# Optimization experiments

Measured on AMD Instinct MI355X. Metric: run time of the kernel, lower is better.

The kernel has to match this reference:

```python
import jax, jax.numpy as jnp
import numpy as np

B, N, K, D, H = 8, 128, 64, 256, 8  # batch, groups, keys-per-query, k_dim (=h_size), n_head


def setup_inputs() -> dict:
    key = jax.random.key(0)
    kq, kk, kv, kw, kb = jax.random.split(key, 5)
    bound = 1.0 / np.sqrt(D)  # torch nn.Bilinear default init bound
    return {
        "q": jax.random.normal(kq, (B, N, 1, D), jnp.float32),
        "k": jax.random.normal(kk, (B, N, K, D), jnp.float32),
        "v": jax.random.normal(kv, (B, N, K, D), jnp.float32),
        "W": jax.random.uniform(kw, (H, D, D), jnp.float32, -bound, bound),
        "b": jax.random.uniform(kb, (H,), jnp.float32, -bound, bound),
    }


def reference(q, k, v, W, b):
    Bs, Ns, Ks, Ds = k.shape
    Hh = W.shape[0]
    qe = q[:, :, 0, :]  # (B,N,D); torch expands q over K, einsum broadcasts instead
    # nn.Bilinear: scores[b,n,k,h] = q[b,n,:] @ W[h] @ k[b,n,k,:] + b[h]
    scores = jnp.einsum('bnd,hde,bnke->bnkh', qe, W, k) + b  # (B,N,K,H)
    # Faithful to torch's .view(B, N, -1, K): row-major reinterpretation of the
    # trailing (K, H) pair as (H, K) — a dim-mixing reshape, not a transpose.
    attn = scores.reshape(Bs, Ns, Hh, Ks)
    attn = jax.nn.softmax(attn, axis=-1)  # softmax over last dim (dropout p=0)
    # matmul(attn, v) -> (B,N,H,Dv); then sum over the head axis
    output = jnp.einsum('bnhk,bnkd->bnd', attn, v)
    return output, attn
```

## Files before the change

kernel.cpp:

```cpp
#include <hip/hip_runtime.h>
#include <math.h>

namespace {

constexpr int D = 256;
constexpr int H = 8;

typedef __attribute__((ext_vector_type(8))) short bf16x8;
typedef __attribute__((ext_vector_type(4))) float f32x4;

__device__ inline unsigned short bf16rn(float x) {
  unsigned u = __builtin_bit_cast(unsigned, x);
  u += 0x7fffu + ((u >> 16) & 1u);
  return (unsigned short)(u >> 16);
}
__device__ inline float bf16tof(unsigned short b) {
  return __builtin_bit_cast(float, (unsigned)b << 16);
}

constexpr size_t OFF_QW  = 0;
constexpr size_t OFF_WFH = (size_t)8 << 20;
constexpr size_t OFF_WFL = (size_t)9 << 20;
constexpr size_t OFF_QFH = (size_t)10 << 20;
constexpr size_t OFF_QFL = ((size_t)10 << 20) + ((size_t)512 << 10);

__global__ __launch_bounds__(256) void prep_kernel(
    const float* __restrict__ q, const float* __restrict__ W,
    char* __restrict__ ws) {
  const int gid = blockIdx.x * 256 + threadIdx.x;
  float e[8];
  char *hi_base, *lo_base;
  size_t outoff;
  if (gid < 65536) {
    const int l = gid & 63, ks = (gid >> 6) & 7, he = gid >> 9;
    const int h = he >> 4, et = he & 15;
    const int d0 = ks * 32 + ((l >> 4) << 3);
    const int ecol = et * 16 + (l & 15);
    const float* src = W + (size_t)h * 65536 + (size_t)d0 * 256 + ecol;
    #pragma unroll
    for (int j = 0; j < 8; ++j) e[j] = src[j * 256];
    hi_base = ws + OFF_WFH; lo_base = ws + OFF_WFL;
    outoff = (size_t)gid * 16;
  } else {
    const int t = gid - 65536;
    const int l = t & 63, ks = (t >> 6) & 7, bt = t >> 9;
    const int row = bt * 16 + (l & 15);
    const int d0 = ks * 32 + ((l >> 4) << 3);
    const float4* src = reinterpret_cast<const float4*>(q + (size_t)row * 256 + d0);
    float4 a = src[0], b = src[1];
    e[0] = a.x; e[1] = a.y; e[2] = a.z; e[3] = a.w;
    e[4] = b.x; e[5] = b.y; e[6] = b.z; e[7] = b.w;
    hi_base = ws + OFF_QFH; lo_base = ws + OFF_QFL;
    outoff = (size_t)t * 16;
  }
  unsigned hw[4], lw[4];
  #pragma unroll
  for (int p = 0; p < 4; ++p) {
    unsigned short h0 = bf16rn(e[2 * p]), h1 = bf16rn(e[2 * p + 1]);
    unsigned short l0 = bf16rn(e[2 * p] - bf16tof(h0));
    unsigned short l1 = bf16rn(e[2 * p + 1] - bf16tof(h1));
    hw[p] = (unsigned)h0 | ((unsigned)h1 << 16);
    lw[p] = (unsigned)l0 | ((unsigned)l1 << 16);
  }
  *reinterpret_cast<uint4*>(hi_base + outoff) = make_uint4(hw[0], hw[1], hw[2], hw[3]);
  *reinterpret_cast<uint4*>(lo_base + outoff) = make_uint4(lw[0], lw[1], lw[2], lw[3]);
}

__global__ __launch_bounds__(256) void qw_mfma_kernel(
    const char* __restrict__ ws_in, float* __restrict__ qW) {
  const int tid = threadIdx.x;
  const int w   = blockIdx.x * 4 + (tid >> 6);
  const int l   = tid & 63;
  const int bng = w >> 5;
  const int heg = w & 31;
  const char* qfh = ws_in + OFF_QFH;
  const char* qfl = ws_in + OFF_QFL;
  const char* wfh = ws_in + OFF_WFH;
  const char* wfl = ws_in + OFF_WFL;

  f32x4 acc[2][4];
  #pragma unroll
  for (int i = 0; i < 2; ++i)
    #pragma unroll
    for (int j = 0; j < 4; ++j) acc[i][j] = {0.f, 0.f, 0.f, 0.f};

  #pragma unroll 2
  for (int ks = 0; ks < 8; ++ks) {
    bf16x8 aH[2], aL[2], bH[4], bL[4];
    #pragma unroll
    for (int i = 0; i < 2; ++i) {
      const size_t off = ((size_t)((bng * 2 + i) * 8 + ks) * 64 + l) * 16;
      aH[i] = *reinterpret_cast<const bf16x8*>(qfh + off);
      aL[i] = *reinterpret_cast<const bf16x8*>(qfl + off);
    }
    #pragma unroll
    for (int j = 0; j < 4; ++j) {
      const size_t off = ((size_t)((heg * 4 + j) * 8 + ks) * 64 + l) * 16;
      bH[j] = *reinterpret_cast<const bf16x8*>(wfh + off);
      bL[j] = *reinterpret_cast<const bf16x8*>(wfl + off);
    }
    #pragma unroll
    for (int i = 0; i < 2; ++i)
      #pragma unroll
      for (int j = 0; j < 4; ++j) {
        acc[i][j] = __builtin_amdgcn_mfma_f32_16x16x32_bf16(aH[i], bH[j], acc[i][j], 0, 0, 0);
        acc[i][j] = __builtin_amdgcn_mfma_f32_16x16x32_bf16(aH[i], bL[j], acc[i][j], 0, 0, 0);
        acc[i][j] = __builtin_amdgcn_mfma_f32_16x16x32_bf16(aL[i], bH[j], acc[i][j], 0, 0, 0);
      }
  }

  const int rbase = (l >> 4) * 4;
  const int col   = l & 15;
  #pragma unroll
  for (int i = 0; i < 2; ++i)
    #pragma unroll
    for (int j = 0; j < 4; ++j) {
      const size_t cidx = (size_t)(heg * 4 + j) * 16 + col;
      #pragma unroll
      for (int r = 0; r < 4; ++r) {
        const int bn = (bng * 2 + i) * 16 + rbase + r;
        qW[(size_t)bn * 2048 + cidx] = acc[i][j][r];
      }
    }
}

constexpr int FA_HI = 0;
constexpr int FA_LO = 16640;
constexpr int FB_HI = 33280;
constexpr int FB_LO = 41600;
constexpr int SMEM_BYTES = 49920;

__global__ __launch_bounds__(256) void score_kernel(
    const float* __restrict__ qW, const float* __restrict__ kin,
    const float* __restrict__ bin, float* __restrict__ attn_out) {
  __shared__ alignas(16) long long smem_ll[SMEM_BYTES / 8];
  char* sm = reinterpret_cast<char*>(smem_ll);
  const int tid = threadIdx.x;
  const int bn  = blockIdx.x;
  const int kh  = blockIdx.y;
  const int wid = tid >> 6;
  const int ln  = tid & 63;

  const float4* k4 = reinterpret_cast<const float4*>(kin) +
                     (size_t)bn * 4096 + (size_t)kh * 2048;
  float4 kv[8];
  #pragma unroll
  for (int i = 0; i < 8; ++i) kv[i] = k4[tid + 256 * i];
  const float4* qw4 = reinterpret_cast<const float4*>(qW) + (size_t)bn * 512;
  float4 qv0 = qw4[tid];
  float4 qv1 = qw4[tid + 256];

  {
    const uint4 z = make_uint4(0u, 0u, 0u, 0u);
    #pragma unroll
    for (int i = 0; i < 2; ++i) {
      int idx = tid + 256 * i;
      int region = idx >> 8;
      int rem = idx & 255;
      int ks = rem >> 5, slot = 32 + (rem & 31);
      int off = (region ? FB_LO : FB_HI) + ks * 1040 + slot * 16;
      *reinterpret_cast<uint4*>(sm + off) = z;
    }
  }

  #pragma unroll
  for (int i = 0; i < 8; ++i) {
    int quad = tid + 256 * i;
    int row = quad >> 6, equad = quad & 63;
    int tile = row >> 4, lrow = row & 15;
    int ks = equad >> 3, g = (equad >> 1) & 3, j0 = (equad & 1) * 4;
    int base = tile * 8320 + ks * 1040 + (lrow * 4 + g) * 16 + j0 * 2;
    float e[4] = {kv[i].x, kv[i].y, kv[i].z, kv[i].w};
    unsigned short h0 = bf16rn(e[0]), h1 = bf16rn(e[1]),
                   h2 = bf16rn(e[2]), h3 = bf16rn(e[3]);
    unsigned short l0 = bf16rn(e[0] - bf16tof(h0)), l1 = bf16rn(e[1] - bf16tof(h1)),
                   l2 = bf16rn(e[2] - bf16tof(h2)), l3 = bf16rn(e[3] - bf16tof(h3));
    uint2 hw = make_uint2((unsigned)h0 | ((unsigned)h1 << 16),
                          (unsigned)h2 | ((unsigned)h3 << 16));
    uint2 lw = make_uint2((unsigned)l0 | ((unsigned)l1 << 16),
                          (unsigned)l2 | ((unsigned)l3 << 16));
    *reinterpret_cast<uint2*>(sm + FA_HI + base) = hw;
    *reinterpret_cast<uint2*>(sm + FA_LO + base) = lw;
  }
  #pragma unroll
  for (int i = 0; i < 2; ++i) {
    int p = tid + 256 * i;
    int hh = p >> 6, equad = p & 63;
    int ks = equad >> 3, g = (equad >> 1) & 3, j0 = (equad & 1) * 4;
    int base = ks * 1040 + (hh * 4 + g) * 16 + j0 * 2;
    float4 qv = i == 0 ? qv0 : qv1;
    float e[4] = {qv.x, qv.y, qv.z, qv.w};
    unsigned short h0 = bf16rn(e[0]), h1 = bf16rn(e[1]),
                   h2 = bf16rn(e[2]), h3 = bf16rn(e[3]);
    unsigned short l0 = bf16rn(e[0] - bf16tof(h0)), l1 = bf16rn(e[1] - bf16tof(h1)),
                   l2 = bf16rn(e[2] - bf16tof(h2)), l3 = bf16rn(e[3] - bf16tof(h3));
    uint2 hw = make_uint2((unsigned)h0 | ((unsigned)h1 << 16),
                          (unsigned)h2 | ((unsigned)h3 << 16));
    uint2 lw = make_uint2((unsigned)l0 | ((unsigned)l1 << 16),
                          (unsigned)l2 | ((unsigned)l3 << 16));
    *reinterpret_cast<uint2*>(sm + FB_HI + base) = hw;
    *reinterpret_cast<uint2*>(sm + FB_LO + base) = lw;
  }
  __syncthreads();
  if (wid >= 2) return;

  const int T = wid;
  const int slot_r = (ln & 15) * 4 + (ln >> 4);
  const char* paH = sm + FA_HI + T * 8320 + slot_r * 16;
  const char* paL = sm + FA_LO + T * 8320 + slot_r * 16;
  const char* pbH = sm + FB_HI + slot_r * 16;
  const char* pbL = sm + FB_LO + slot_r * 16;
  f32x4 acc = {0.f, 0.f, 0.f, 0.f};
  #pragma unroll
  for (int ks = 0; ks < 8; ++ks) {
    bf16x8 aH = *reinterpret_cast<const bf16x8*>(paH + ks * 1040);
    bf16x8 aL = *reinterpret_cast<const bf16x8*>(paL + ks * 1040);
    bf16x8 bH = *reinterpret_cast<const bf16x8*>(pbH + ks * 1040);
    bf16x8 bL = *reinterpret_cast<const bf16x8*>(pbL + ks * 1040);
    acc = __builtin_amdgcn_mfma_f32_16x16x32_bf16(aH, bH, acc, 0, 0, 0);
    acc = __builtin_amdgcn_mfma_f32_16x16x32_bf16(aH, bL, acc, 0, 0, 0);
    acc = __builtin_amdgcn_mfma_f32_16x16x32_bf16(aL, bH, acc, 0, 0, 0);
  }

  const int col = ln & 15;
  const bool valid = col < 8;
  const float bias = bin[ln & 7];
  float x0 = acc[0] + bias, x1 = acc[1] + bias, x2 = acc[2] + bias, x3 = acc[3] + bias;
  float m = valid ? fmaxf(fmaxf(x0, x1), fmaxf(x2, x3)) : -1e30f;
  m = fmaxf(m, __shfl_xor(m, 1, 64));
  m = fmaxf(m, __shfl_xor(m, 2, 64));
  m = fmaxf(m, __shfl_xor(m, 4, 64));
  m = fmaxf(m, __shfl_xor(m, 16, 64));
  float e0 = valid ? expf(x0 - m) : 0.f;
  float e1 = valid ? expf(x1 - m) : 0.f;
  float e2 = valid ? expf(x2 - m) : 0.f;
  float e3 = valid ? expf(x3 - m) : 0.f;
  float s = e0 + e1 + e2 + e3;
  s += __shfl_xor(s, 1, 64);
  s += __shfl_xor(s, 2, 64);
  s += __shfl_xor(s, 4, 64);
  s += __shfl_xor(s, 16, 64);
  if (valid) {
    float inv = 1.f / s;
    size_t base = (size_t)bn * 512 + (size_t)(kh * 32 + T * 16 + (ln >> 4) * 4) * 8 + col;
    attn_out[base]      = e0 * inv;
    attn_out[base + 8]  = e1 * inv;
    attn_out[base + 16] = e2 * inv;
    attn_out[base + 24] = e3 * inv;
  }
}

__global__ __launch_bounds__(256) void pv_kernel(
    const float* __restrict__ vin, const float* __restrict__ attn_in,
    float* __restrict__ out) {
  __shared__ float wpart[4][64];
  __shared__ float wsum[64];
  __shared__ float s_red[4][260];
  const int tid = threadIdx.x;
  const int bn  = blockIdx.x;
  const int wid = tid >> 6;
  const int ln  = tid & 63;

  float a0 = attn_in[(size_t)bn * 512 + tid];
  float a1 = attn_in[(size_t)bn * 512 + 256 + tid];
  wpart[wid][ln] = a0 + a1;
  __syncthreads();
  if (tid < 64) wsum[tid] = wpart[0][tid] + wpart[1][tid] + wpart[2][tid] + wpart[3][tid];
  __syncthreads();

  const float4* v4 = reinterpret_cast<const float4*>(vin) + (size_t)bn * 4096;
  float4 acc = make_float4(0.f, 0.f, 0.f, 0.f);
  #pragma unroll 8
  for (int i = 0; i < 16; ++i) {
    const int r = wid + 4 * i;
    float w = wsum[r];
    float4 vv = v4[r * 64 + ln];
    acc.x += w * vv.x; acc.y += w * vv.y; acc.z += w * vv.z; acc.w += w * vv.w;
  }
  *reinterpret_cast<float4*>(&s_red[wid][ln << 2]) = acc;
  __syncthreads();

  out[(size_t)bn * D + tid] =
      s_red[0][tid] + s_red[1][tid] + s_red[2][tid] + s_red[3][tid];
}

}

extern "C" void kernel_launch(void* const* d_in, const int* in_sizes, int n_in,
                              void* d_out, int out_size, void* d_ws, size_t ws_size,
                              hipStream_t stream) {
  const float* q = (const float*)d_in[0];
  const float* k = (const float*)d_in[1];
  const float* v = (const float*)d_in[2];
  const float* W = (const float*)d_in[3];
  const float* b = (const float*)d_in[4];

  float* out  = (float*)d_out;
  float* attn = out + 262144;
  char*  ws   = (char*)d_ws;
  float* qWbuf = (float*)(ws + OFF_QW);

  hipLaunchKernelGGL(prep_kernel,    dim3(384), dim3(256), 0, stream, q, W, ws);
  hipLaunchKernelGGL(qw_mfma_kernel, dim3(256), dim3(256), 0, stream, ws, qWbuf);
  hipLaunchKernelGGL(score_kernel,   dim3(1024, 2), dim3(256), 0, stream,
                     qWbuf, k, b, attn);
  hipLaunchKernelGGL(pv_kernel,      dim3(1024), dim3(256), 0, stream,
                     v, attn, out);
}
```

Baseline: 47.47 us.

## Fuse score and PV kernels into one per-group kernel with prefetched k/v

Merges the score/softmax kernel and the PV reduction kernel into a single kernel with one block per (b,n). Each block handles both key halves in sequence, and the second half of k and all of v are loaded into registers during the first half's MFMA phase. Column sums of attention are accumulated in shared memory instead of being re-read from global. This removes one launch and the global round trip of attn, and overlaps the loads with compute. In exchange there are half as many blocks, with more registers and shared memory per block, which may lower occupancy and parallelism.

```diff
diff --git a/kernel.cpp b/kernel.cpp
--- a/kernel.cpp
+++ b/kernel.cpp
@@ -128,25 +128,29 @@
 constexpr int FA_LO = 16640;
 constexpr int FB_HI = 33280;
 constexpr int FB_LO = 41600;
-constexpr int SMEM_BYTES = 49920;
-
-__global__ __launch_bounds__(256) void score_kernel(
+constexpr int WSP_OFF = 49920;
+constexpr int SMEM2 = 50432;
+
+__global__ __launch_bounds__(256) void attn_fused_kernel(
     const float* __restrict__ qW, const float* __restrict__ kin,
-    const float* __restrict__ bin, float* __restrict__ attn_out) {
-  __shared__ alignas(16) long long smem_ll[SMEM_BYTES / 8];
+    const float* __restrict__ vin, const float* __restrict__ bin,
+    float* __restrict__ out, float* __restrict__ attn_out) {
+  __shared__ alignas(16) long long smem_ll[SMEM2 / 8];
   char* sm = reinterpret_cast<char*>(smem_ll);
+  float* wsp = reinterpret_cast<float*>(sm + WSP_OFF);
   const int tid = threadIdx.x;
   const int bn  = blockIdx.x;
-  const int kh  = blockIdx.y;
   const int wid = tid >> 6;
   const int ln  = tid & 63;
 
-  const float4* k4 = reinterpret_cast<const float4*>(kin) +
-                     (size_t)bn * 4096 + (size_t)kh * 2048;
-  float4 kv[8];
-  #pragma unroll
-  for (int i = 0; i < 8; ++i) kv[i] = k4[tid + 256 * i];
+  const float4* k4  = reinterpret_cast<const float4*>(kin) + (size_t)bn * 4096;
+  const float4* v4  = reinterpret_cast<const float4*>(vin) + (size_t)bn * 4096;
   const float4* qw4 = reinterpret_cast<const float4*>(qW) + (size_t)bn * 512;
+  const float bias = bin[ln & 7];
+
+  float4 kv1[8];
+  #pragma unroll
+  for (int i = 0; i < 8; ++i) kv1[i] = k4[tid + 256 * i];
   float4 qv0 = qw4[tid];
   float4 qv1 = qw4[tid + 256];
 
@@ -163,25 +167,29 @@
     }
   }
 
-  #pragma unroll
-  for (int i = 0; i < 8; ++i) {
-    int quad = tid + 256 * i;
-    int row = quad >> 6, equad = quad & 63;
-    int tile = row >> 4, lrow = row & 15;
-    int ks = equad >> 3, g = (equad >> 1) & 3, j0 = (equad & 1) * 4;
-    int base = tile * 8320 + ks * 1040 + (lrow * 4 + g) * 16 + j0 * 2;
-    float e[4] = {kv[i].x, kv[i].y, kv[i].z, kv[i].w};
-    unsigned short h0 = bf16rn(e[0]), h1 = bf16rn(e[1]),
-                   h2 = bf16rn(e[2]), h3 = bf16rn(e[3]);
-    unsigned short l0 = bf16rn(e[0] - bf16tof(h0)), l1 = bf16rn(e[1] - bf16tof(h1)),
-                   l2 = bf16rn(e[2] - bf16tof(h2)), l3 = bf16rn(e[3] - bf16tof(h3));
-    uint2 hw = make_uint2((unsigned)h0 | ((unsigned)h1 << 16),
-                          (unsigned)h2 | ((unsigned)h3 << 16));
-    uint2 lw = make_uint2((unsigned)l0 | ((unsigned)l1 << 16),
-                          (unsigned)l2 | ((unsigned)l3 << 16));
-    *reinterpret_cast<uint2*>(sm + FA_HI + base) = hw;
-    *reinterpret_cast<uint2*>(sm + FA_LO + base) = lw;
-  }
+  auto convert_k = [&](const float4* kv) {
+    #pragma unroll
+    for (int i = 0; i < 8; ++i) {
+      int quad = tid + 256 * i;
+      int row = quad >> 6, equad = quad & 63;
+      int tile = row >> 4, lrow = row & 15;
+      int ks = equad >> 3, g = (equad >> 1) & 3, j0 = (equad & 1) * 4;
+      int base = tile * 8320 + ks * 1040 + (lrow * 4 + g) * 16 + j0 * 2;
+      float e[4] = {kv[i].x, kv[i].y, kv[i].z, kv[i].w};
+      unsigned short h0 = bf16rn(e[0]), h1 = bf16rn(e[1]),
+                     h2 = bf16rn(e[2]), h3 = bf16rn(e[3]);
+      unsigned short l0 = bf16rn(e[0] - bf16tof(h0)), l1 = bf16rn(e[1] - bf16tof(h1)),
+                     l2 = bf16rn(e[2] - bf16tof(h2)), l3 = bf16rn(e[3] - bf16tof(h3));
+      uint2 hw = make_uint2((unsigned)h0 | ((unsigned)h1 << 16),
+                            (unsigned)h2 | ((unsigned)h3 << 16));
+      uint2 lw = make_uint2((unsigned)l0 | ((unsigned)l1 << 16),
+                            (unsigned)l2 | ((unsigned)l3 << 16));
+      *reinterpret_cast<uint2*>(sm + FA_HI + base) = hw;
+      *reinterpret_cast<uint2*>(sm + FA_LO + base) = lw;
+    }
+  };
+
+  convert_k(kv1);
   #pragma unroll
   for (int i = 0; i < 2; ++i) {
     int p = tid + 256 * i;
@@ -201,87 +209,116 @@
     *reinterpret_cast<uint2*>(sm + FB_HI + base) = hw;
     *reinterpret_cast<uint2*>(sm + FB_LO + base) = lw;
   }
-  __syncthreads();
-  if (wid >= 2) return;
-
-  const int T = wid;
-  const int slot_r = (ln & 15) * 4 + (ln >> 4);
-  const char* paH = sm + FA_HI + T * 8320 + slot_r * 16;
-  const char* paL = sm + FA_LO + T * 8320 + slot_r * 16;
-  const char* pbH = sm + FB_HI + slot_r * 16;
-  const char* pbL = sm + FB_LO + slot_r * 16;
-  f32x4 acc = {0.f, 0.f, 0.f, 0.f};
-  #pragma unroll
-  for (int ks = 0; ks < 8; ++ks) {
-    bf16x8 aH = *reinterpret_cast<const bf16x8*>(paH + ks * 1040);
-    bf16x8 aL = *reinterpret_cast<const bf16x8*>(paL + ks * 1040);
-    bf16x8 bH = *reinterpret_cast<const bf16x8*>(pbH + ks * 1040);
-    bf16x8 bL = *reinterpret_cast<const bf16x8*>(pbL + ks * 1040);
-    acc = __builtin_amdgcn_mfma_f32_16x16x32_bf16(aH, bH, acc, 0, 0, 0);
-    acc = __builtin_amdgcn_mfma_f32_16x16x32_bf16(aH, bL, acc, 0, 0, 0);
-    acc = __builtin_amdgcn_mfma_f32_16x16x32_bf16(aL, bH, acc, 0, 0, 0);
-  }
-
-  const int col = ln & 15;
-  const bool valid = col < 8;
-  const float bias = bin[ln & 7];
-  float x0 = acc[0] + bias, x1 = acc[1] + bias, x2 = acc[2] + bias, x3 = acc[3] + bias;
-  float m = valid ? fmaxf(fmaxf(x0, x1), fmaxf(x2, x3)) : -1e30f;
-  m = fmaxf(m, __shfl_xor(m, 1, 64));
-  m = fmaxf(m, __shfl_xor(m, 2, 64));
-  m = fmaxf(m, __shfl_xor(m, 4, 64));
-  m = fmaxf(m, __shfl_xor(m, 16, 64));
-  float e0 = valid ? expf(x0 - m) : 0.f;
-  float e1 = valid ? expf(x1 - m) : 0.f;
-  float e2 = valid ? expf(x2 - m) : 0.f;
-  float e3 = valid ? expf(x3 - m) : 0.f;
-  float s = e0 + e1 + e2 + e3;
-  s += __shfl_xor(s, 1, 64);
-  s += __shfl_xor(s, 2, 64);
-  s += __shfl_xor(s, 4, 64);
-  s += __shfl_xor(s, 16, 64);
-  if (valid) {
+
+  float4 kv2[8];
+  #pragma unroll
+  for (int i = 0; i < 8; ++i) kv2[i] = k4[2048 + tid + 256 * i];
+  float4 vva[8];
+  #pragma unroll
+  for (int i = 0; i < 8; ++i) vva[i] = v4[(wid + 4 * i) * 64 + ln];
+  __builtin_amdgcn_sched_barrier(0);
+  __syncthreads();
+
+  auto do_phase = [&](int kh, bool first) {
+    const int T = wid;
+    const int slot_r = (ln & 15) * 4 + (ln >> 4);
+    const char* paH = sm + FA_HI + T * 8320 + slot_r * 16;
+    const char* paL = sm + FA_LO + T * 8320 + slot_r * 16;
+    const char* pbH = sm + FB_HI + slot_r * 16;
+    const char* pbL = sm + FB_LO + slot_r * 16;
+    f32x4 acc = {0.f, 0.f, 0.f, 0.f};
+    #pragma unroll
+    for (int ks = 0; ks < 8; ++ks) {
+      bf16x8 aH = *reinterpret_cast<const bf16x8*>(paH + ks * 1040);
+      bf16x8 aL = *reinterpret_cast<const bf16x8*>(paL + ks * 1040);
+      bf16x8 bH = *reinterpret_cast<const bf16x8*>(pbH + ks * 1040);
+      bf16x8 bL = *reinterpret_cast<const bf16x8*>(pbL + ks * 1040);
+      acc = __builtin_amdgcn_mfma_f32_16x16x32_bf16(aH, bH, acc, 0, 0, 0);
+      acc = __builtin_amdgcn_mfma_f32_16x16x32_bf16(aH, bL, acc, 0, 0, 0);
+      acc = __builtin_amdgcn_mfma_f32_16x16x32_bf16(aL, bH, acc, 0, 0, 0);
+    }
+    const int col = ln & 15;
+    const bool valid = col < 8;
+    float x0 = acc[0] + bias, x1 = acc[1] + bias, x2 = acc[2] + bias, x3 = acc[3] + bias;
+    float m = valid ? fmaxf(fmaxf(x0, x1), fmaxf(x2, x3)) : -1e30f;
+    m = fmaxf(m, __shfl_xor(m, 1, 64));
+    m = fmaxf(m, __shfl_xor(m, 2, 64));
+    m = fmaxf(m, __shfl_xor(m, 4, 64));
+    m = fmaxf(m, __shfl_xor(m, 16, 64));
+    float e0 = valid ? expf(x0 - m) : 0.f;
+    float e1 = valid ? expf(x1 - m) : 0.f;
+    float e2 = valid ? expf(x2 - m) : 0.f;
+    float e3 = valid ? expf(x3 - m) : 0.f;
+    float s = e0 + e1 + e2 + e3;
+    s += __shfl_xor(s, 1, 64);
+    s += __shfl_xor(s, 2, 64);
+    s += __shfl_xor(s, 4, 64);
+    s += __shfl_xor(s, 16, 64);
     float inv = 1.f / s;
-    size_t base = (size_t)bn * 512 + (size_t)(kh * 32 + T * 16 + (ln >> 4) * 4) * 8 + col;
-    attn_out[base]      = e0 * inv;
-    attn_out[base + 8]  = e1 * inv;
-    attn_out[base + 16] = e2 * inv;
-    attn_out[base + 24] = e3 * inv;
-  }
-}
-
-__global__ __launch_bounds__(256) void pv_kernel(
-    const float* __restrict__ vin, const float* __restrict__ attn_in,
-    float* __restrict__ out) {
-  __shared__ float wpart[4][64];
-  __shared__ float wsum[64];
-  __shared__ float s_red[4][260];
-  const int tid = threadIdx.x;
-  const int bn  = blockIdx.x;
-  const int wid = tid >> 6;
-  const int ln  = tid & 63;
-
-  float a0 = attn_in[(size_t)bn * 512 + tid];
-  float a1 = attn_in[(size_t)bn * 512 + 256 + tid];
-  wpart[wid][ln] = a0 + a1;
-  __syncthreads();
-  if (tid < 64) wsum[tid] = wpart[0][tid] + wpart[1][tid] + wpart[2][tid] + wpart[3][tid];
-  __syncthreads();
-
-  const float4* v4 = reinterpret_cast<const float4*>(vin) + (size_t)bn * 4096;
+    float p0 = e0 * inv, p1 = e1 * inv, p2 = e2 * inv, p3 = e3 * inv;
+    if (valid) {
+      size_t base = (size_t)bn * 512 + (size_t)(kh * 32 + T * 16 + (ln >> 4) * 4) * 8 + col;
+      attn_out[base]      = p0;
+      attn_out[base + 8]  = p1;
+      attn_out[base + 16] = p2;
+      attn_out[base + 24] = p3;
+    }
+    p0 += __shfl_xor(p0, 32, 64);
+    p1 += __shfl_xor(p1, 32, 64);
+    p2 += __shfl_xor(p2, 32, 64);
+    p3 += __shfl_xor(p3, 32, 64);
+    if (ln < 32 && (ln & 15) < 8) {
+      const int rb = (ln >> 4) * 4;
+      const int c8 = ln & 7;
+      float* w = wsp + T * 64;
+      if (first) {
+        w[(rb + 0) * 8 + c8] = p0;
+        w[(rb + 1) * 8 + c8] = p1;
+        w[(rb + 2) * 8 + c8] = p2;
+        w[(rb + 3) * 8 + c8] = p3;
+      } else {
+        w[(rb + 0) * 8 + c8] += p0;
+        w[(rb + 1) * 8 + c8] += p1;
+        w[(rb + 2) * 8 + c8] += p2;
+        w[(rb + 3) * 8 + c8] += p3;
+      }
+    }
+  };
+
+  if (wid < 2) do_phase(0, true);
+  __syncthreads();
+
+  convert_k(kv2);
+  float4 vvb[8];
+  #pragma unroll
+  for (int i = 0; i < 8; ++i) vvb[i] = v4[(32 + wid + 4 * i) * 64 + ln];
+  __builtin_amdgcn_sched_barrier(0);
+  __syncthreads();
+
+  if (wid < 2) do_phase(1, false);
+  __syncthreads();
+
   float4 acc = make_float4(0.f, 0.f, 0.f, 0.f);
-  #pragma unroll 8
-  for (int i = 0; i < 16; ++i) {
+  #pragma unroll
+  for (int i = 0; i < 8; ++i) {
     const int r = wid + 4 * i;
-    float w = wsum[r];
-    float4 vv = v4[r * 64 + ln];
-    acc.x += w * vv.x; acc.y += w * vv.y; acc.z += w * vv.z; acc.w += w * vv.w;
-  }
-  *reinterpret_cast<float4*>(&s_red[wid][ln << 2]) = acc;
+    float w = wsp[r] + wsp[64 + r];
+    acc.x += w * vva[i].x; acc.y += w * vva[i].y;
+    acc.z += w * vva[i].z; acc.w += w * vva[i].w;
+  }
+  #pragma unroll
+  for (int i = 0; i < 8; ++i) {
+    const int r = 32 + wid + 4 * i;
+    float w = wsp[r] + wsp[64 + r];
+    acc.x += w * vvb[i].x; acc.y += w * vvb[i].y;
+    acc.z += w * vvb[i].z; acc.w += w * vvb[i].w;
+  }
+  float* s_red = reinterpret_cast<float*>(sm);
+  *reinterpret_cast<float4*>(&s_red[wid * 260 + (ln << 2)]) = acc;
   __syncthreads();
 
   out[(size_t)bn * D + tid] =
-      s_red[0][tid] + s_red[1][tid] + s_red[2][tid] + s_red[3][tid];
+      s_red[tid] + s_red[260 + tid] + s_red[520 + tid] + s_red[780 + tid];
 }
 
 }
@@ -300,10 +337,8 @@
   char*  ws   = (char*)d_ws;
   float* qWbuf = (float*)(ws + OFF_QW);
 
-  hipLaunchKernelGGL(prep_kernel,    dim3(384), dim3(256), 0, stream, q, W, ws);
-  hipLaunchKernelGGL(qw_mfma_kernel, dim3(256), dim3(256), 0, stream, ws, qWbuf);
-  hipLaunchKernelGGL(score_kernel,   dim3(1024, 2), dim3(256), 0, stream,
-                     qWbuf, k, b, attn);
-  hipLaunchKernelGGL(pv_kernel,      dim3(1024), dim3(256), 0, stream,
-                     v, attn, out);
-}
+  hipLaunchKernelGGL(prep_kernel,       dim3(384),  dim3(256), 0, stream, q, W, ws);
+  hipLaunchKernelGGL(qw_mfma_kernel,    dim3(256),  dim3(256), 0, stream, ws, qWbuf);
+  hipLaunchKernelGGL(attn_fused_kernel, dim3(1024), dim3(256), 0, stream,
+                     qWbuf, k, v, b, out, attn);
+}
```

Measured after the change: 44.70 us. -5.8%, faster.
